# Kernel tuning notes

Hardware: AMD Instinct MI355X
Metric: run time of the kernel (lower is better)

## Reference

```python
import jax, jax.numpy as jnp
import numpy as np

N = 50000      # nodes
E = 800000     # edges
IN = 128       # in_dim
EMB = 32       # emb_dim
ED = 8         # edge_dim
L = 4          # num_layers
B = 64         # num graphs in batch
OUT = 10       # out_dim
EPS = 1e-5


def setup_inputs() -> dict:
    key = jax.random.key(0)
    ks = jax.random.split(key, 16)
    f32 = jnp.float32
    def nrm(k, shape, scale):
        return jax.random.normal(k, shape, dtype=f32) * scale
    inp = {}
    inp['x'] = nrm(ks[0], (N, IN), 1.0)
    inp['edge_index'] = jax.random.randint(ks[1], (2, E), 0, N)
    inp['edge_attr'] = nrm(ks[2], (E, ED), 1.0)
    inp['batch'] = jnp.sort(jax.random.randint(ks[3], (N,), 0, B))
    # lin_in
    inp['lin_in_w'] = nrm(ks[4], (IN, EMB), 0.05)
    inp['lin_in_b'] = jnp.zeros((EMB,), f32)
    # per-layer message MLP: Linear(2e+ed->e), BN, ReLU, Linear(e->e), BN, ReLU
    inp['msg_w1'] = nrm(ks[5], (L, 2 * EMB + ED, EMB), 0.1)
    inp['msg_b1'] = jnp.zeros((L, EMB), f32)
    inp['msg_g1'] = jnp.ones((L, EMB), f32)
    inp['msg_be1'] = jnp.zeros((L, EMB), f32)
    inp['msg_w2'] = nrm(ks[6], (L, EMB, EMB), 0.1)
    inp['msg_b2'] = jnp.zeros((L, EMB), f32)
    inp['msg_g2'] = jnp.ones((L, EMB), f32)
    inp['msg_be2'] = jnp.zeros((L, EMB), f32)
    # per-layer update MLP: Linear(2e->e), BN, ReLU, Linear(e->e), BN, ReLU
    inp['upd_w1'] = nrm(ks[7], (L, 2 * EMB, EMB), 0.1)
    inp['upd_b1'] = jnp.zeros((L, EMB), f32)
    inp['upd_g1'] = jnp.ones((L, EMB), f32)
    inp['upd_be1'] = jnp.zeros((L, EMB), f32)
    inp['upd_w2'] = nrm(ks[8], (L, EMB, EMB), 0.1)
    inp['upd_b2'] = jnp.zeros((L, EMB), f32)
    inp['upd_g2'] = jnp.ones((L, EMB), f32)
    inp['upd_be2'] = jnp.zeros((L, EMB), f32)
    # lin_pred
    inp['pred_w'] = nrm(ks[9], (EMB, OUT), 0.1)
    inp['pred_b'] = jnp.zeros((OUT,), f32)
    return inp


def _bn(x, g, b):
    # BatchNorm1d in training mode: batch stats over dim 0 (biased variance)
    mu = jnp.mean(x, axis=0)
    var = jnp.mean(jnp.square(x - mu), axis=0)
    return (x - mu) * jax.lax.rsqrt(var + EPS) * g + b


def reference(x, edge_attr, lin_in_w, lin_in_b,
              msg_w1, msg_b1, msg_g1, msg_be1, msg_w2, msg_b2, msg_g2, msg_be2,
              upd_w1, upd_b1, upd_g1, upd_be1, upd_w2, upd_b2, upd_g2, upd_be2,
              pred_w, pred_b, edge_index, batch):
    src = edge_index[0]  # h_j source nodes
    dst = edge_index[1]  # h_i target nodes (aggregation index)
    h = x @ lin_in_w + lin_in_b  # [N, EMB]
    for i in range(L):
        # message: gather + concat + MLP(BN,ReLU)x2 over edges
        msg_in = jnp.concatenate([h[dst], h[src], edge_attr], axis=-1)  # [E, 2e+ed]
        m = jax.nn.relu(_bn(msg_in @ msg_w1[i] + msg_b1[i], msg_g1[i], msg_be1[i]))
        m = jax.nn.relu(_bn(m @ msg_w2[i] + msg_b2[i], msg_g2[i], msg_be2[i]))
        # aggregate: scatter-add by destination
        aggr = jax.ops.segment_sum(m, dst, num_segments=N)  # [N, EMB]
        # update: concat + MLP(BN,ReLU)x2
        u = jnp.concatenate([h, aggr], axis=-1)  # [N, 2e]
        u = jax.nn.relu(_bn(u @ upd_w1[i] + upd_b1[i], upd_g1[i], upd_be1[i]))
        u = jax.nn.relu(_bn(u @ upd_w2[i] + upd_b2[i], upd_g2[i], upd_be2[i]))
        h = u + h  # residual in MPNNModel.get_embeddings
    # global mean pool
    sums = jax.ops.segment_sum(h, batch, num_segments=B)
    counts = jax.ops.segment_sum(jnp.ones((N,), h.dtype), batch, num_segments=B)
    h_graph = sums / jnp.maximum(counts, 1.0)[:, None]
    return h_graph @ pred_w + pred_b  # [B, OUT]
```

## Files before the change

kernel.cpp:

```cpp
#include <hip/hip_runtime.h>
#include <cstddef>

#define N_NODES 50000
#define N_EDGES 800000
#define IN_DIM  128
#define EMB     32
#define ED      8
#define NLAYERS 4
#define NB      64
#define OUTD    10
#define EPS_BN  1e-5f

#define EDGE_GRID 3125
#define NODE_GRID 196
#define NODE4_GRID 782
#define AU_GRID   6250
#define NTILE_N   3125
#define LIN_GRID  782
#define ST_TPW    4
#define ST_GRID   3125
#define MSG2_TPW  4
#define MSG2_GRID 3125

#define SREP 4

typedef short bf16x8 __attribute__((ext_vector_type(8)));
typedef float f32x4  __attribute__((ext_vector_type(4)));


__device__ __forceinline__ unsigned short f2bf(float x) {
  union { float f; unsigned u; } v; v.f = x;
  unsigned b = v.u + 0x7FFFu + ((v.u >> 16) & 1u);
  return (unsigned short)(b >> 16);
}
__device__ __forceinline__ float bf2f(unsigned short s) {
  union { unsigned u; float f; } v; v.u = ((unsigned)s) << 16;
  return v.f;
}

__device__ __forceinline__ void coef_from_stats(const float* __restrict__ stats_stage,
                                                const float* __restrict__ g,
                                                const float* __restrict__ be,
                                                float inv_count, float* __restrict__ cf) {
  if (threadIdx.x < EMB) {
    const int c = threadIdx.x;
    float s = 0.f, ss = 0.f;
#pragma unroll
    for (int r = 0; r < SREP; ++r) {
      s  += stats_stage[r*64 + c];
      ss += stats_stage[r*64 + EMB + c];
    }
    const float mu  = s * inv_count;
    const float var = ss * inv_count - mu*mu;
    const float a = g[c] * rsqrtf(var + EPS_BN);
    cf[c] = a;
    cf[EMB + c] = fmaf(-mu, a, be[c]);
  }
  __syncthreads();
}

__device__ __forceinline__ void wave_stats_atomic(float ts[8], float tss[8],
                                                  float* __restrict__ lds_s,
                                                  float* __restrict__ lds_q,
                                                  float* __restrict__ stats_stage) {
  const int lane = threadIdx.x & 63;
  const int wv   = threadIdx.x >> 6;
#pragma unroll
  for (int j = 0; j < 8; ++j) {
    float a = ts[j], b = tss[j];
#pragma unroll
    for (int o = 32; o > 0; o >>= 1) {
      a += __shfl_down(a, o, 64);
      b += __shfl_down(b, o, 64);
    }
    ts[j] = a; tss[j] = b;
  }
  if (lane == 0) {
#pragma unroll
    for (int j = 0; j < 8; ++j) {
      lds_s[wv*8 + j] = ts[j];
      lds_q[wv*8 + j] = tss[j];
    }
  }
  __syncthreads();
  if (threadIdx.x < 64) {
    const float v = (threadIdx.x < 32) ? lds_s[threadIdx.x] : lds_q[threadIdx.x - 32];
    atomicAdd(stats_stage + ((blockIdx.x & (SREP-1)) << 6) + threadIdx.x, v);
  }
}

#define HSTRIDE 40

__global__ __launch_bounds__(256) void k_lin_in_pq(
    const float* __restrict__ x, const float* __restrict__ w, const float* __restrict__ b,
    const float* __restrict__ w1, const float* __restrict__ b1, const int* __restrict__ ei,
    float* __restrict__ h, unsigned short* __restrict__ p, unsigned short* __restrict__ q,
    int* __restrict__ cnt)
{
  __shared__ __align__(16) unsigned short lds_hb[4][16*HSTRIDE];
  __shared__ __align__(16) unsigned short lds_pq[4][16*HSTRIDE];
  const int lane = threadIdx.x & 63;
  const int wv   = threadIdx.x >> 6;
  const int n0i  = lane & 15;
  const int quad = lane >> 4;

  const int tile = blockIdx.x*4 + wv;
  if (tile < NTILE_N) {
    const int r0 = tile*16;
    bf16x8 BwL[4], BwH[4];
#pragma unroll
    for (int kb = 0; kb < 4; ++kb) {
#pragma unroll
      for (int j = 0; j < 8; ++j) {
        const int k = kb*32 + quad*8 + j;
        BwL[kb][j] = (short)f2bf(w[k*EMB + n0i]);
        BwH[kb][j] = (short)f2bf(w[k*EMB + 16 + n0i]);
      }
    }
    f32x4 accL = {0.f,0.f,0.f,0.f};
    f32x4 accH = {0.f,0.f,0.f,0.f};
#pragma unroll
    for (int kb = 0; kb < 4; ++kb) {
      const float4 xa = *(const float4*)(x + (size_t)(r0 + n0i)*IN_DIM + kb*32 + quad*8);
      const float4 xb = *(const float4*)(x + (size_t)(r0 + n0i)*IN_DIM + kb*32 + quad*8 + 4);
      bf16x8 A;
      A[0] = (short)f2bf(xa.x); A[1] = (short)f2bf(xa.y);
      A[2] = (short)f2bf(xa.z); A[3] = (short)f2bf(xa.w);
      A[4] = (short)f2bf(xb.x); A[5] = (short)f2bf(xb.y);
      A[6] = (short)f2bf(xb.z); A[7] = (short)f2bf(xb.w);
      accL = __builtin_amdgcn_mfma_f32_16x16x32_bf16(A, BwL[kb], accL, 0, 0, 0);
      accH = __builtin_amdgcn_mfma_f32_16x16x32_bf16(A, BwH[kb], accH, 0, 0, 0);
    }
    const float bL = b[n0i], bH = b[16 + n0i];
#pragma unroll
    for (int r = 0; r < 4; ++r) {
      const int row = quad*4 + r;
      const float vL = accL[r] + bL;
      const float vH = accH[r] + bH;
      h[(size_t)(r0 + row)*EMB + n0i]      = vL;
      h[(size_t)(r0 + row)*EMB + 16 + n0i] = vH;
      lds_hb[wv][row*HSTRIDE + n0i]      = f2bf(vL);
      lds_hb[wv][row*HSTRIDE + 16 + n0i] = f2bf(vH);
    }
    bf16x8 A2;
#pragma unroll
    for (int j = 0; j < 8; ++j)
      A2[j] = (short)lds_hb[wv][n0i*HSTRIDE + quad*8 + j];
    bf16x8 BpL, BpH, BqL, BqH;
#pragma unroll
    for (int j = 0; j < 8; ++j) {
      const int k = quad*8 + j;
      BpL[j] = (short)f2bf(w1[k*EMB + n0i]);
      BpH[j] = (short)f2bf(w1[k*EMB + 16 + n0i]);
      BqL[j] = (short)f2bf(w1[(EMB + k)*EMB + n0i]);
      BqH[j] = (short)f2bf(w1[(EMB + k)*EMB + 16 + n0i]);
    }
    const f32x4 z4 = {0.f,0.f,0.f,0.f};
    f32x4 pL = __builtin_amdgcn_mfma_f32_16x16x32_bf16(A2, BpL, z4, 0, 0, 0);
    f32x4 pH = __builtin_amdgcn_mfma_f32_16x16x32_bf16(A2, BpH, z4, 0, 0, 0);
    f32x4 qL = __builtin_amdgcn_mfma_f32_16x16x32_bf16(A2, BqL, z4, 0, 0, 0);
    f32x4 qH = __builtin_amdgcn_mfma_f32_16x16x32_bf16(A2, BqH, z4, 0, 0, 0);
    const float b1L = b1[n0i], b1H = b1[16 + n0i];
#pragma unroll
    for (int r = 0; r < 4; ++r) {
      const int row = quad*4 + r;
      lds_pq[wv][row*HSTRIDE + n0i]      = f2bf(pL[r] + b1L);
      lds_pq[wv][row*HSTRIDE + 16 + n0i] = f2bf(pH[r] + b1H);
    }
    {
      const int row2 = lane >> 2;
      const int c8   = (lane & 3)*8;
      const uint4 ov = *(const uint4*)&lds_pq[wv][row2*HSTRIDE + c8];
      *(uint4*)(p + (size_t)(r0 + row2)*EMB + c8) = ov;
    }
#pragma unroll
    for (int r = 0; r < 4; ++r) {
      const int row = quad*4 + r;
      lds_pq[wv][row*HSTRIDE + n0i]      = f2bf(qL[r]);
      lds_pq[wv][row*HSTRIDE + 16 + n0i] = f2bf(qH[r]);
    }
    {
      const int row2 = lane >> 2;
      const int c8   = (lane & 3)*8;
      const uint4 ov = *(const uint4*)&lds_pq[wv][row2*HSTRIDE + c8];
      *(uint4*)(q + (size_t)(r0 + row2)*EMB + c8) = ov;
    }
  }
  for (int e = blockIdx.x*256 + threadIdx.x; e < N_EDGES; e += gridDim.x*256)
    atomicAdd(&cnt[ei[N_EDGES + e]], 1);
}

__global__ __launch_bounds__(256) void k_scan_a(const int* __restrict__ cnt,
                                                int* __restrict__ row_ptr, int* __restrict__ bsum) {
  __shared__ int s[256];
  const int gid = blockIdx.x*256 + threadIdx.x;
  const int v = (gid < N_NODES) ? cnt[gid] : 0;
  s[threadIdx.x] = v;
  __syncthreads();
  for (int o = 1; o < 256; o <<= 1) {
    const int t = (threadIdx.x >= o) ? s[threadIdx.x - o] : 0;
    __syncthreads();
    s[threadIdx.x] += t;
    __syncthreads();
  }
  if (gid < N_NODES) row_ptr[gid] = s[threadIdx.x] - v;
  if (threadIdx.x == 255) bsum[blockIdx.x] = s[255];
}

__global__ __launch_bounds__(256) void k_scan_bc(int* __restrict__ row_ptr,
                                                 const int* __restrict__ bsum) {
  __shared__ int s[256];
  const int t = threadIdx.x;
  const int v = (t < NODE_GRID) ? bsum[t] : 0;
  s[t] = v;
  __syncthreads();
  for (int o = 1; o < 256; o <<= 1) {
    const int tt = (t >= o) ? s[t - o] : 0;
    __syncthreads();
    s[t] += tt;
    __syncthreads();
  }
  const int off = (blockIdx.x == 0) ? 0 : s[blockIdx.x - 1];
  const int gid = blockIdx.x*256 + t;
  if (gid < N_NODES) row_ptr[gid] += off;
  if (blockIdx.x == 0 && t == 0) row_ptr[N_NODES] = N_EDGES;
}

__global__ __launch_bounds__(256) void k_place_scatter(
    const int* __restrict__ ei, const float* __restrict__ ea,
    const int* __restrict__ row_ptr, int* __restrict__ cnt2,
    uint4* __restrict__ rec)
{
  const int e = blockIdx.x*256 + threadIdx.x;
  const int s = ei[e];
  const int d = ei[N_EDGES + e];
  const int pos = row_ptr[d] + atomicAdd(&cnt2[d], 1);
  const float4 v0 = ((const float4*)(ea + (size_t)e*ED))[0];
  const float4 v1 = ((const float4*)(ea + (size_t)e*ED))[1];
  const float ev[8] = {v0.x, v0.y, v0.z, v0.w, v1.x, v1.y, v1.z, v1.w};
  unsigned u[4];
#pragma unroll
  for (int j = 0; j < 4; ++j)
    u[j] = (unsigned)f2bf(ev[2*j]) | ((unsigned)f2bf(ev[2*j+1]) << 16);
  uint4* rp = rec + (size_t)pos*2;
  rp[0] = make_uint4((unsigned)s, (unsigned)d, u[0], u[1]);
  rp[1] = make_uint4(u[2], u[3], 0u, 0u);
}


__global__ __launch_bounds__(256) void k_stats1(
    const unsigned short* __restrict__ pb, const unsigned short* __restrict__ qb,
    const uint4* __restrict__ rec, const float* __restrict__ w1b,
    float* __restrict__ stats)
{
  __shared__ float lds_d[4][16*33];
  __shared__ float lds_s[4][32], lds_q[4][32];
  const int lane = threadIdx.x & 63;
  const int wv   = threadIdx.x >> 6;
  const int l15  = lane & 15;
  const int quad = lane >> 4;

  bf16x8 B1lo = {}, B1hi = {};
  if (quad == 0) {
#pragma unroll
    for (int j = 0; j < 8; ++j) {
      B1lo[j] = (short)f2bf(w1b[j*EMB + l15]);
      B1hi[j] = (short)f2bf(w1b[j*EMB + 16 + l15]);
    }
  }

  const int tile0 = blockIdx.x * (4*ST_TPW);
  uint4 RA[ST_TPW], RB[ST_TPW];
#pragma unroll
  for (int t = 0; t < ST_TPW; ++t) {
    const int tile = tile0 + t*4 + wv;
    const size_t e0 = (size_t)tile * 16;
    const uint4* r4 = rec + (e0 + l15)*2;
    RA[t] = r4[0];
    RB[t] = (quad == 0) ? r4[1] : make_uint4(0u,0u,0u,0u);
  }
  uint4 PG[ST_TPW], QG[ST_TPW];
#pragma unroll
  for (int t = 0; t < ST_TPW; ++t) {
    PG[t] = *(const uint4*)(pb + (size_t)RA[t].y*EMB + quad*8);
    QG[t] = *(const uint4*)(qb + (size_t)RA[t].x*EMB + quad*8);
  }

  float ts[8], tss[8];
#pragma unroll
  for (int j = 0; j < 8; ++j) { ts[j] = 0.f; tss[j] = 0.f; }

#pragma unroll
  for (int t = 0; t < ST_TPW; ++t) {
    bf16x8 A = {};
    if (quad == 0) {
      A[0] = (short)(RA[t].z & 0xFFFFu); A[1] = (short)(RA[t].z >> 16);
      A[2] = (short)(RA[t].w & 0xFFFFu); A[3] = (short)(RA[t].w >> 16);
      A[4] = (short)(RB[t].x & 0xFFFFu); A[5] = (short)(RB[t].x >> 16);
      A[6] = (short)(RB[t].y & 0xFFFFu); A[7] = (short)(RB[t].y >> 16);
    }
    const f32x4 z4 = {0.f,0.f,0.f,0.f};
    f32x4 D0 = __builtin_amdgcn_mfma_f32_16x16x32_bf16(A, B1lo, z4, 0, 0, 0);
    f32x4 D1 = __builtin_amdgcn_mfma_f32_16x16x32_bf16(A, B1hi, z4, 0, 0, 0);
#pragma unroll
    for (int r = 0; r < 4; ++r) {
      const int row = quad*4 + r;
      lds_d[wv][row*33 + l15]      = D0[r];
      lds_d[wv][row*33 + 16 + l15] = D1[r];
    }
    const unsigned pu[4] = {PG[t].x, PG[t].y, PG[t].z, PG[t].w};
    const unsigned qu[4] = {QG[t].x, QG[t].y, QG[t].z, QG[t].w};
#pragma unroll
    for (int jj = 0; jj < 4; ++jj) {
      const float d0 = lds_d[wv][l15*33 + quad*8 + 2*jj];
      const float d1 = lds_d[wv][l15*33 + quad*8 + 2*jj + 1];
      const float v0 = (d0 + bf2f((unsigned short)(pu[jj] & 0xFFFFu)))
                            + bf2f((unsigned short)(qu[jj] & 0xFFFFu));
      const float v1 = (d1 + bf2f((unsigned short)(pu[jj] >> 16)))
                            + bf2f((unsigned short)(qu[jj] >> 16));
      const float w0 = bf2f(f2bf(v0));
      const float w1v = bf2f(f2bf(v1));
      ts[2*jj]   += w0;  tss[2*jj]   = fmaf(w0, w0, tss[2*jj]);
      ts[2*jj+1] += w1v; tss[2*jj+1] = fmaf(w1v, w1v, tss[2*jj+1]);
    }
  }

#pragma unroll
  for (int j = 0; j < 8; ++j) {
    float a = ts[j], b = tss[j];
#pragma unroll
    for (int o = 1; o < 16; o <<= 1) {
      a += __shfl_xor(a, o, 64);
      b += __shfl_xor(b, o, 64);
    }
    ts[j] = a; tss[j] = b;
  }
  if (l15 == 0) {
#pragma unroll
    for (int j = 0; j < 8; ++j) {
      lds_s[wv][quad*8 + j] = ts[j];
      lds_q[wv][quad*8 + j] = tss[j];
    }
  }
  __syncthreads();
  if (threadIdx.x < 64) {
    const int c = threadIdx.x & 31;
    const int kind = threadIdx.x >> 5;
    float v = 0.f;
#pragma unroll
    for (int wq = 0; wq < 4; ++wq)
      v += kind ? lds_q[wq][c] : lds_s[wq][c];
    atomicAdd(stats + ((blockIdx.x & (SREP-1)) << 6) + kind*32 + c, v);
  }
}

__global__ __launch_bounds__(256) void k_msg2(
    const unsigned short* __restrict__ pb, const unsigned short* __restrict__ qb,
    const uint4* __restrict__ rec, const float* __restrict__ w1b,
    const float* __restrict__ stats1, const float* __restrict__ g1, const float* __restrict__ be1,
    const float* __restrict__ w2, const float* __restrict__ b2,
    unsigned short* __restrict__ y, float* __restrict__ stats2)
{
  __shared__ float lds_d[4][16*33];
  __shared__ __align__(16) unsigned short lds_t[4][16*32];
  __shared__ float lds_s[4][32], lds_q[4][32];
  __shared__ float cf[64];

  coef_from_stats(stats1, g1, be1, 1.0f/(float)N_EDGES, cf);

  const int lane = threadIdx.x & 63;
  const int wv   = threadIdx.x >> 6;
  const int l15  = lane & 15;
  const int quad = lane >> 4;

  bf16x8 B1lo = {}, B1hi = {};
  if (quad == 0) {
#pragma unroll
    for (int j = 0; j < 8; ++j) {
      B1lo[j] = (short)f2bf(w1b[j*EMB + l15]);
      B1hi[j] = (short)f2bf(w1b[j*EMB + 16 + l15]);
    }
  }
  bf16x8 Blo, Bhi;
#pragma unroll
  for (int j = 0; j < 8; ++j) {
    Blo[j] = (short)f2bf(w2[(quad*8 + j)*EMB + l15]);
    Bhi[j] = (short)f2bf(w2[(quad*8 + j)*EMB + 16 + l15]);
  }
  float a1[8], c1[8];
#pragma unroll
  for (int j = 0; j < 8; ++j) {
    a1[j] = cf[quad*8 + j];
    c1[j] = cf[EMB + quad*8 + j];
  }
  const float b2c0 = b2[l15], b2c1 = b2[16 + l15];

  float ts[8], tss[8];
#pragma unroll
  for (int j = 0; j < 8; ++j) { ts[j] = 0.f; tss[j] = 0.f; }

  const int tile0 = blockIdx.x * (4*MSG2_TPW);

  uint4 cRA, cRB, cPG, cQG;
  {
    const size_t e0 = (size_t)(tile0 + wv) * 16;
    const uint4* r4 = rec + (e0 + l15)*2;
    cRA = r4[0];
    cRB = (quad == 0) ? r4[1] : make_uint4(0u,0u,0u,0u);
    cPG = *(const uint4*)(pb + (size_t)cRA.y*EMB + quad*8);
    cQG = *(const uint4*)(qb + (size_t)cRA.x*EMB + quad*8);
  }

#pragma unroll
  for (int t = 0; t < MSG2_TPW; ++t) {
    const size_t e0 = (size_t)(tile0 + t*4 + wv) * 16;

    uint4 nRA = make_uint4(0u,0u,0u,0u), nRB = make_uint4(0u,0u,0u,0u);
    uint4 nPG = make_uint4(0u,0u,0u,0u), nQG = make_uint4(0u,0u,0u,0u);
    if (t + 1 < MSG2_TPW) {
      const size_t e1 = (size_t)(tile0 + (t+1)*4 + wv) * 16;
      const uint4* r4 = rec + (e1 + l15)*2;
      nRA = r4[0];
      nRB = (quad == 0) ? r4[1] : make_uint4(0u,0u,0u,0u);
    }

    bf16x8 A = {};
    if (quad == 0) {
      A[0] = (short)(cRA.z & 0xFFFFu); A[1] = (short)(cRA.z >> 16);
      A[2] = (short)(cRA.w & 0xFFFFu); A[3] = (short)(cRA.w >> 16);
      A[4] = (short)(cRB.x & 0xFFFFu); A[5] = (short)(cRB.x >> 16);
      A[6] = (short)(cRB.y & 0xFFFFu); A[7] = (short)(cRB.y >> 16);
    }
    const f32x4 z4 = {0.f,0.f,0.f,0.f};
    f32x4 D0 = __builtin_amdgcn_mfma_f32_16x16x32_bf16(A, B1lo, z4, 0, 0, 0);
    f32x4 D1 = __builtin_amdgcn_mfma_f32_16x16x32_bf16(A, B1hi, z4, 0, 0, 0);
#pragma unroll
    for (int r = 0; r < 4; ++r) {
      const int row = quad*4 + r;
      lds_d[wv][row*33 + l15]      = D0[r];
      lds_d[wv][row*33 + 16 + l15] = D1[r];
    }

    if (t + 1 < MSG2_TPW) {
      nPG = *(const uint4*)(pb + (size_t)nRA.y*EMB + quad*8);
      nQG = *(const uint4*)(qb + (size_t)nRA.x*EMB + quad*8);
    }

    const unsigned pu[4] = {cPG.x, cPG.y, cPG.z, cPG.w};
    const unsigned qu[4] = {cQG.x, cQG.y, cQG.z, cQG.w};
    bf16x8 A2;
#pragma unroll
    for (int jj = 0; jj < 4; ++jj) {
      const float d0 = lds_d[wv][l15*33 + quad*8 + 2*jj];
      const float d1 = lds_d[wv][l15*33 + quad*8 + 2*jj + 1];
      const float v0 = (d0 + bf2f((unsigned short)(pu[jj] & 0xFFFFu)))
                            + bf2f((unsigned short)(qu[jj] & 0xFFFFu));
      const float v1 = (d1 + bf2f((unsigned short)(pu[jj] >> 16)))
                            + bf2f((unsigned short)(qu[jj] >> 16));
      const float w0 = bf2f(f2bf(v0));
      const float w1v = bf2f(f2bf(v1));
      const float r0 = fmaxf(fmaf(a1[2*jj],   w0,  c1[2*jj]),   0.f);
      const float r1 = fmaxf(fmaf(a1[2*jj+1], w1v, c1[2*jj+1]), 0.f);
      A2[2*jj]   = (short)f2bf(r0);
      A2[2*jj+1] = (short)f2bf(r1);
    }

    f32x4 acc0 = {0.f, 0.f, 0.f, 0.f};
    f32x4 acc1 = {0.f, 0.f, 0.f, 0.f};
    acc0 = __builtin_amdgcn_mfma_f32_16x16x32_bf16(A2, Blo, acc0, 0, 0, 0);
    acc1 = __builtin_amdgcn_mfma_f32_16x16x32_bf16(A2, Bhi, acc1, 0, 0, 0);

#pragma unroll
    for (int r = 0; r < 4; ++r) {
      const int row = quad*4 + r;
      lds_t[wv][row*32 + l15]      = f2bf(acc0[r] + b2c0);
      lds_t[wv][row*32 + 16 + l15] = f2bf(acc1[r] + b2c1);
    }
    const uint4 orow = *(const uint4*)&lds_t[wv][(lane>>2)*32 + (lane&3)*8];
    *(uint4*)(y + (e0 + (lane>>2))*EMB + (lane&3)*8) = orow;

    const unsigned uo[4] = {orow.x, orow.y, orow.z, orow.w};
#pragma unroll
    for (int j = 0; j < 4; ++j) {
      const float v0 = bf2f((unsigned short)(uo[j] & 0xFFFFu));
      const float v1 = bf2f((unsigned short)(uo[j] >> 16));
      ts[2*j]   += v0;  tss[2*j]   = fmaf(v0, v0, tss[2*j]);
      ts[2*j+1] += v1;  tss[2*j+1] = fmaf(v1, v1, tss[2*j+1]);
    }

    cRA = nRA; cRB = nRB; cPG = nPG; cQG = nQG;
  }

#pragma unroll
  for (int j = 0; j < 8; ++j) {
    float s = ts[j], qq = tss[j];
#pragma unroll
    for (int o = 4; o < 64; o <<= 1) {
      s  += __shfl_xor(s, o, 64);
      qq += __shfl_xor(qq, o, 64);
    }
    ts[j] = s; tss[j] = qq;
  }
  if (lane < 4) {
#pragma unroll
    for (int j = 0; j < 8; ++j) {
      lds_s[wv][lane*8 + j] = ts[j];
      lds_q[wv][lane*8 + j] = tss[j];
    }
  }
  __syncthreads();
  if (threadIdx.x < 64) {
    const int c = threadIdx.x & 31;
    const int kind = threadIdx.x >> 5;
    float v = 0.f;
#pragma unroll
    for (int wq = 0; wq < 4; ++wq)
      v += kind ? lds_q[wq][c] : lds_s[wq][c];
    atomicAdd(stats2 + ((blockIdx.x & (SREP-1)) << 6) + kind*32 + c, v);
  }
}

__global__ __launch_bounds__(256) void k_aggr_upd1(
    const unsigned short* __restrict__ y, const int* __restrict__ row_ptr,
    const float* __restrict__ h,
    const float* __restrict__ stats1, const float* __restrict__ g2, const float* __restrict__ be2,
    const float* __restrict__ uw1, const float* __restrict__ ub1,
    float* __restrict__ z, float* __restrict__ stats2)
{
  __shared__ float cf[64];
  __shared__ float lh[8][32];
  __shared__ float la[8][32];
  __shared__ float rs[4][32], rq[4][32];
  coef_from_stats(stats1, g2, be2, 1.0f/(float)N_EDGES, cf);

  const int g = threadIdx.x >> 5;
  const int l = threadIdx.x & 31;
  const int n = blockIdx.x*8 + g;

  lh[g][l] = h[(size_t)n*EMB + l];

  const int c8  = (l & 3) * 8;
  const int rof = l >> 2;
  float a[8], b[8];
#pragma unroll
  for (int j = 0; j < 8; ++j) { a[j] = cf[c8 + j]; b[j] = cf[EMB + c8 + j]; }
  const int lo = row_ptr[n], hi = row_ptr[n+1];
  float acc[8];
#pragma unroll
  for (int j = 0; j < 8; ++j) acc[j] = 0.f;
  for (int r = lo + rof; r < hi; r += 8) {
    const uint4 u = *(const uint4*)(y + (size_t)r*EMB + c8);
    const unsigned uu[4] = {u.x, u.y, u.z, u.w};
#pragma unroll
    for (int t = 0; t < 4; ++t) {
      const float v0 = bf2f((unsigned short)(uu[t] & 0xFFFFu));
      const float v1 = bf2f((unsigned short)(uu[t] >> 16));
      acc[2*t]   += fmaxf(fmaf(a[2*t],   v0, b[2*t]),   0.f);
      acc[2*t+1] += fmaxf(fmaf(a[2*t+1], v1, b[2*t+1]), 0.f);
    }
  }
#pragma unroll
  for (int j = 0; j < 8; ++j) {
    float v = acc[j];
    v += __shfl_xor(v, 4, 64);
    v += __shfl_xor(v, 8, 64);
    v += __shfl_xor(v, 16, 64);
    acc[j] = v;
  }
  if (rof == 0) {
#pragma unroll
    for (int j = 0; j < 8; ++j) la[g][c8 + j] = acc[j];
  }
  __syncthreads();

  float accu = ub1[l];
#pragma unroll
  for (int k = 0; k < EMB; ++k) accu = fmaf(lh[g][k], uw1[k*EMB + l], accu);
#pragma unroll
  for (int k = 0; k < EMB; ++k) accu = fmaf(la[g][k], uw1[(EMB + k)*EMB + l], accu);
  z[(size_t)n*EMB + l] = accu;

  const float sq = accu*accu;
  const float a2 = accu + __shfl_down(accu, 32, 64);
  const float q2 = sq   + __shfl_down(sq,   32, 64);
  const int wv = threadIdx.x >> 6;
  if ((threadIdx.x & 63) < 32) { rs[wv][l] = a2; rq[wv][l] = q2; }
  __syncthreads();
  if (threadIdx.x < 64) {
    const int c = threadIdx.x & 31;
    const int kind = threadIdx.x >> 5;
    float v = 0.f;
#pragma unroll
    for (int wq = 0; wq < 4; ++wq)
      v += kind ? rq[wq][c] : rs[wq][c];
    atomicAdd(stats2 + ((blockIdx.x & (SREP-1)) << 6) + kind*32 + c, v);
  }
}

__global__ __launch_bounds__(256) void k_upd2(
    float* __restrict__ z,
    const float* __restrict__ stats1, const float* __restrict__ g1, const float* __restrict__ be1,
    const float* __restrict__ w, const float* __restrict__ b,
    float* __restrict__ stats2)
{
  __shared__ float cf[64];
  __shared__ float lds_s[32], lds_q[32];
  coef_from_stats(stats1, g1, be1, 1.0f/(float)N_NODES, cf);

  const int lane = threadIdx.x & 63;
  const int wv   = threadIdx.x >> 6;
  const int n  = blockIdx.x*64 + lane;
  const int c0 = wv*8;
  float acc[8];
#pragma unroll
  for (int j = 0; j < 8; ++j) acc[j] = 0.f;
  if (n < N_NODES) {
#pragma unroll
    for (int j = 0; j < 8; ++j) acc[j] = b[c0 + j];
    const float4* zp = (const float4*)(z + (size_t)n*EMB);
#pragma unroll
    for (int k4 = 0; k4 < 8; ++k4) {
      const float4 v = zp[k4];
      const float mv[4] = {v.x, v.y, v.z, v.w};
#pragma unroll
      for (int t = 0; t < 4; ++t) {
        const int k = 4*k4 + t;
        const float m = fmaxf(fmaf(cf[k], mv[t], cf[EMB + k]), 0.f);
        const float* wk = w + k*EMB + c0;
#pragma unroll
        for (int j = 0; j < 8; ++j) acc[j] = fmaf(m, wk[j], acc[j]);
      }
    }
  }
  float ts[8], tss[8];
#pragma unroll
  for (int j = 0; j < 8; ++j) { ts[j] = acc[j]; tss[j] = acc[j]*acc[j]; }
  wave_stats_atomic(ts, tss, lds_s, lds_q, stats2);
  if (n < N_NODES) {
    float4 o0, o1;
    o0.x = acc[0]; o0.y = acc[1]; o0.z = acc[2]; o0.w = acc[3];
    o1.x = acc[4]; o1.y = acc[5]; o1.z = acc[6]; o1.w = acc[7];
    *(float4*)(z + (size_t)n*EMB + c0)     = o0;
    *(float4*)(z + (size_t)n*EMB + c0 + 4) = o1;
  }
}

__global__ __launch_bounds__(256) void k_resid_pq(
    float* __restrict__ h, const float* __restrict__ z,
    const float* __restrict__ stats, const float* __restrict__ g, const float* __restrict__ be,
    const float* __restrict__ w1_next, const float* __restrict__ b1_next,
    unsigned short* __restrict__ p, unsigned short* __restrict__ q)
{
  __shared__ float cf[64];
  __shared__ float lds_h[64][33];
  coef_from_stats(stats, g, be, 1.0f/(float)N_NODES, cf);

  const int lane = threadIdx.x & 63;
  const int wv   = threadIdx.x >> 6;
  const int n  = blockIdx.x*64 + lane;
  const int c0 = wv*8;
  if (n < N_NODES) {
    const float4* zp = (const float4*)(z + (size_t)n*EMB + c0);
    float4* hp = (float4*)(h + (size_t)n*EMB + c0);
    float hn[8];
    const float4 z0 = zp[0], z1 = zp[1];
    const float4 h0 = hp[0], h1 = hp[1];
    const float zv[8] = {z0.x, z0.y, z0.z, z0.w, z1.x, z1.y, z1.z, z1.w};
    const float hv[8] = {h0.x, h0.y, h0.z, h0.w, h1.x, h1.y, h1.z, h1.w};
#pragma unroll
    for (int j = 0; j < 8; ++j) {
      const int k = c0 + j;
      hn[j] = hv[j] + fmaxf(fmaf(cf[k], zv[j], cf[EMB + k]), 0.f);
      lds_h[lane][k] = hn[j];
    }
    float4 o0, o1;
    o0.x = hn[0]; o0.y = hn[1]; o0.z = hn[2]; o0.w = hn[3];
    o1.x = hn[4]; o1.y = hn[5]; o1.z = hn[6]; o1.w = hn[7];
    hp[0] = o0; hp[1] = o1;
  }
  __syncthreads();
  if (n < N_NODES && w1_next) {
    float ap[8], aq[8];
#pragma unroll
    for (int j = 0; j < 8; ++j) { ap[j] = b1_next[c0 + j]; aq[j] = 0.f; }
#pragma unroll
    for (int k = 0; k < EMB; ++k) {
      const float hvv = lds_h[lane][k];
      const float* wp = w1_next + k*EMB + c0;
      const float* wq = w1_next + (EMB + k)*EMB + c0;
#pragma unroll
      for (int j = 0; j < 8; ++j) ap[j] = fmaf(hvv, wp[j], ap[j]);
#pragma unroll
      for (int j = 0; j < 8; ++j) aq[j] = fmaf(hvv, wq[j], aq[j]);
    }
    unsigned up[4], uq[4];
#pragma unroll
    for (int j = 0; j < 4; ++j) {
      up[j] = (unsigned)f2bf(ap[2*j]) | ((unsigned)f2bf(ap[2*j+1]) << 16);
      uq[j] = (unsigned)f2bf(aq[2*j]) | ((unsigned)f2bf(aq[2*j+1]) << 16);
    }
    uint4 op; op.x = up[0]; op.y = up[1]; op.z = up[2]; op.w = up[3];
    uint4 oq; oq.x = uq[0]; oq.y = uq[1]; oq.z = uq[2]; oq.w = uq[3];
    *(uint4*)(p + (size_t)n*EMB + c0) = op;
    *(uint4*)(q + (size_t)n*EMB + c0) = oq;
  }
}

__global__ void k_pool(const float* __restrict__ h, const int* __restrict__ batch,
                       const float* __restrict__ pw, const float* __restrict__ pb,
                       float* __restrict__ out)
{
  __shared__ float sred[256];
  __shared__ float hg[EMB];
  const int b = blockIdx.x;
  int lo = 0, hi = N_NODES;
  while (lo < hi) { int m = (lo + hi) >> 1; if (batch[m] < b) lo = m + 1; else hi = m; }
  const int start = lo;
  hi = N_NODES;
  while (lo < hi) { int m = (lo + hi) >> 1; if (batch[m] < b + 1) lo = m + 1; else hi = m; }
  const int end = lo;

  const int c = threadIdx.x & (EMB-1);
  const int r = threadIdx.x >> 5;
  float s = 0.f;
  for (int n = start + r; n < end; n += 8) s += h[(size_t)n*EMB + c];
  sred[threadIdx.x] = s;
  __syncthreads();
  if (threadIdx.x < EMB) {
    float tot = 0.f;
#pragma unroll
    for (int r2 = 0; r2 < 8; ++r2) tot += sred[r2*EMB + threadIdx.x];
    const float cnt = (float)(end - start);
    hg[threadIdx.x] = tot / fmaxf(cnt, 1.f);
  }
  __syncthreads();
  if (threadIdx.x < OUTD) {
    float acc = pb[threadIdx.x];
#pragma unroll
    for (int cc = 0; cc < EMB; ++cc) acc = fmaf(hg[cc], pw[cc*OUTD + threadIdx.x], acc);
    out[b*OUTD + threadIdx.x] = acc;
  }
}


extern "C" void kernel_launch(void* const* d_in, const int* in_sizes, int n_in,
                              void* d_out, int out_size, void* d_ws, size_t ws_size,
                              hipStream_t stream) {
  const float* x        = (const float*)d_in[0];
  const int*   ei       = (const int*)  d_in[1];
  const float* ea       = (const float*)d_in[2];
  const int*   batch    = (const int*)  d_in[3];
  const float* lin_in_w = (const float*)d_in[4];
  const float* lin_in_b = (const float*)d_in[5];
  const float* msg_w1   = (const float*)d_in[6];
  const float* msg_b1   = (const float*)d_in[7];
  const float* msg_g1   = (const float*)d_in[8];
  const float* msg_be1  = (const float*)d_in[9];
  const float* msg_w2   = (const float*)d_in[10];
  const float* msg_b2   = (const float*)d_in[11];
  const float* msg_g2   = (const float*)d_in[12];
  const float* msg_be2  = (const float*)d_in[13];
  const float* upd_w1   = (const float*)d_in[14];
  const float* upd_b1   = (const float*)d_in[15];
  const float* upd_g1   = (const float*)d_in[16];
  const float* upd_be1  = (const float*)d_in[17];
  const float* upd_w2   = (const float*)d_in[18];
  const float* upd_b2   = (const float*)d_in[19];
  const float* upd_g2   = (const float*)d_in[20];
  const float* upd_be2  = (const float*)d_in[21];
  const float* pred_w   = (const float*)d_in[22];
  const float* pred_b   = (const float*)d_in[23];
  float* out = (float*)d_out;

  char* wsb = (char*)d_ws;
  unsigned short* y  = (unsigned short*)wsb;
  uint4* rec = (uint4*)(wsb + (size_t)N_EDGES*EMB*2);
  unsigned short* p  = (unsigned short*)(rec + (size_t)N_EDGES*2);
  unsigned short* q  = p + (size_t)N_NODES*EMB;
  float* h       = (float*)(q + (size_t)N_NODES*EMB);
  float* z       = h + (size_t)N_NODES*EMB;
  float* stats   = z + (size_t)N_NODES*EMB;
  int*   cnt     = (int*)(stats + 16*SREP*64);
  int*   cnt2    = cnt + N_NODES;
  int*   row_ptr = cnt2 + N_NODES;
  int*   bsum    = row_ptr + N_NODES + 1;
  const size_t need = ((size_t)((char*)(bsum + 256) - wsb));
  if (ws_size < need) return;

  hipMemsetAsync(stats, 0, (16*SREP*64 + 2*N_NODES)*sizeof(float), stream);

  k_lin_in_pq<<<LIN_GRID, 256, 0, stream>>>(x, lin_in_w, lin_in_b, msg_w1, msg_b1, ei,
                                            h, p, q, cnt);
  k_scan_a<<<NODE_GRID, 256, 0, stream>>>(cnt, row_ptr, bsum);
  k_scan_bc<<<NODE_GRID, 256, 0, stream>>>(row_ptr, bsum);
  k_place_scatter<<<EDGE_GRID, 256, 0, stream>>>(ei, ea, row_ptr, cnt2, rec);

  for (int l = 0; l < NLAYERS; ++l) {
    const int st = l*4;
    const float* w1  = msg_w1 + (size_t)l*(2*EMB+ED)*EMB;
    const float* w1b = w1 + (size_t)2*EMB*EMB;
    const float* w2  = msg_w2 + (size_t)l*EMB*EMB;
    const float* uw1 = upd_w1 + (size_t)l*(2*EMB)*EMB;
    const float* uw2 = upd_w2 + (size_t)l*EMB*EMB;
    const float* w1_next = (l+1 < NLAYERS) ? msg_w1 + (size_t)(l+1)*(2*EMB+ED)*EMB : nullptr;
    const float* b1_next = (l+1 < NLAYERS) ? msg_b1 + (size_t)(l+1)*EMB : nullptr;

    k_stats1<<<ST_GRID, 256, 0, stream>>>(p, q, rec, w1b, stats + (size_t)st*SREP*64);
    k_msg2<<<MSG2_GRID, 256, 0, stream>>>(p, q, rec, w1b,
                                          stats + (size_t)st*SREP*64,
                                          msg_g1 + l*EMB, msg_be1 + l*EMB,
                                          w2, msg_b2 + l*EMB,
                                          y, stats + (size_t)(st+1)*SREP*64);
    k_aggr_upd1<<<AU_GRID, 256, 0, stream>>>(y, row_ptr, h,
                                             stats + (size_t)(st+1)*SREP*64,
                                             msg_g2 + l*EMB, msg_be2 + l*EMB,
                                             uw1, upd_b1 + l*EMB,
                                             z, stats + (size_t)(st+2)*SREP*64);
    k_upd2<<<NODE4_GRID, 256, 0, stream>>>(z, stats + (size_t)(st+2)*SREP*64,
                                           upd_g1 + l*EMB, upd_be1 + l*EMB,
                                           uw2, upd_b2 + l*EMB, stats + (size_t)(st+3)*SREP*64);
    k_resid_pq<<<NODE4_GRID, 256, 0, stream>>>(h, z, stats + (size_t)(st+3)*SREP*64,
                                               upd_g2 + l*EMB, upd_be2 + l*EMB,
                                               w1_next, b1_next, p, q);
  }

  k_pool<<<NB, 256, 0, stream>>>(h, batch, pred_w, pred_b, out);
}
```

Before: 820.2 us.

## Keep edge records in original order and aggregate via inverse permutation

Edge records (src, dst, bf16 edge attributes) are now built in original edge order inside the lin_in kernel, instead of being scattered into dst-sorted positions in a separate pass. The placement kernel now only writes an inverse permutation array, and the aggregation kernel reads each message row through that index. The x loads in lin_in are also hoisted ahead of the weight conversion. This saves the scattered 32-byte record writes during preprocessing. In exchange, the per-layer message kernels lose the dst locality of sorted records, and aggregation becomes an indirect gather of message rows.

```diff
diff --git a/kernel.cpp b/kernel.cpp
--- a/kernel.cpp
+++ b/kernel.cpp
@@ -94,8 +94,9 @@
 __global__ __launch_bounds__(256) void k_lin_in_pq(
     const float* __restrict__ x, const float* __restrict__ w, const float* __restrict__ b,
     const float* __restrict__ w1, const float* __restrict__ b1, const int* __restrict__ ei,
+    const float* __restrict__ ea,
     float* __restrict__ h, unsigned short* __restrict__ p, unsigned short* __restrict__ q,
-    int* __restrict__ cnt)
+    int* __restrict__ cnt, uint4* __restrict__ rec)
 {
   __shared__ __align__(16) unsigned short lds_hb[4][16*HSTRIDE];
   __shared__ __align__(16) unsigned short lds_pq[4][16*HSTRIDE];
@@ -107,6 +108,12 @@
   const int tile = blockIdx.x*4 + wv;
   if (tile < NTILE_N) {
     const int r0 = tile*16;
+    float4 xa[4], xb[4];
+#pragma unroll
+    for (int kb = 0; kb < 4; ++kb) {
+      xa[kb] = *(const float4*)(x + (size_t)(r0 + n0i)*IN_DIM + kb*32 + quad*8);
+      xb[kb] = *(const float4*)(x + (size_t)(r0 + n0i)*IN_DIM + kb*32 + quad*8 + 4);
+    }
     bf16x8 BwL[4], BwH[4];
 #pragma unroll
     for (int kb = 0; kb < 4; ++kb) {
@@ -121,13 +128,11 @@
     f32x4 accH = {0.f,0.f,0.f,0.f};
 #pragma unroll
     for (int kb = 0; kb < 4; ++kb) {
-      const float4 xa = *(const float4*)(x + (size_t)(r0 + n0i)*IN_DIM + kb*32 + quad*8);
-      const float4 xb = *(const float4*)(x + (size_t)(r0 + n0i)*IN_DIM + kb*32 + quad*8 + 4);
       bf16x8 A;
-      A[0] = (short)f2bf(xa.x); A[1] = (short)f2bf(xa.y);
-      A[2] = (short)f2bf(xa.z); A[3] = (short)f2bf(xa.w);
-      A[4] = (short)f2bf(xb.x); A[5] = (short)f2bf(xb.y);
-      A[6] = (short)f2bf(xb.z); A[7] = (short)f2bf(xb.w);
+      A[0] = (short)f2bf(xa[kb].x); A[1] = (short)f2bf(xa[kb].y);
+      A[2] = (short)f2bf(xa[kb].z); A[3] = (short)f2bf(xa[kb].w);
+      A[4] = (short)f2bf(xb[kb].x); A[5] = (short)f2bf(xb[kb].y);
+      A[6] = (short)f2bf(xb[kb].z); A[7] = (short)f2bf(xb[kb].w);
       accL = __builtin_amdgcn_mfma_f32_16x16x32_bf16(A, BwL[kb], accL, 0, 0, 0);
       accH = __builtin_amdgcn_mfma_f32_16x16x32_bf16(A, BwH[kb], accH, 0, 0, 0);
     }
@@ -186,8 +191,21 @@
       *(uint4*)(q + (size_t)(r0 + row2)*EMB + c8) = ov;
     }
   }
-  for (int e = blockIdx.x*256 + threadIdx.x; e < N_EDGES; e += gridDim.x*256)
-    atomicAdd(&cnt[ei[N_EDGES + e]], 1);
+  for (int e = blockIdx.x*256 + threadIdx.x; e < N_EDGES; e += gridDim.x*256) {
+    const int s = ei[e];
+    const int d = ei[N_EDGES + e];
+    atomicAdd(&cnt[d], 1);
+    const float4 v0 = ((const float4*)(ea + (size_t)e*ED))[0];
+    const float4 v1 = ((const float4*)(ea + (size_t)e*ED))[1];
+    const float ev[8] = {v0.x, v0.y, v0.z, v0.w, v1.x, v1.y, v1.z, v1.w};
+    unsigned u[4];
+#pragma unroll
+    for (int j = 0; j < 4; ++j)
+      u[j] = (unsigned)f2bf(ev[2*j]) | ((unsigned)f2bf(ev[2*j+1]) << 16);
+    uint4* rp = rec + (size_t)e*2;
+    rp[0] = make_uint4((unsigned)s, (unsigned)d, u[0], u[1]);
+    rp[1] = make_uint4(u[2], u[3], 0u, 0u);
+  }
 }
 
 __global__ __launch_bounds__(256) void k_scan_a(const int* __restrict__ cnt,
@@ -226,25 +244,14 @@
   if (blockIdx.x == 0 && t == 0) row_ptr[N_NODES] = N_EDGES;
 }
 
-__global__ __launch_bounds__(256) void k_place_scatter(
-    const int* __restrict__ ei, const float* __restrict__ ea,
-    const int* __restrict__ row_ptr, int* __restrict__ cnt2,
-    uint4* __restrict__ rec)
+__global__ __launch_bounds__(256) void k_place(
+    const int* __restrict__ ei, const int* __restrict__ row_ptr, int* __restrict__ cnt2,
+    int* __restrict__ inv)
 {
   const int e = blockIdx.x*256 + threadIdx.x;
-  const int s = ei[e];
   const int d = ei[N_EDGES + e];
   const int pos = row_ptr[d] + atomicAdd(&cnt2[d], 1);
-  const float4 v0 = ((const float4*)(ea + (size_t)e*ED))[0];
-  const float4 v1 = ((const float4*)(ea + (size_t)e*ED))[1];
-  const float ev[8] = {v0.x, v0.y, v0.z, v0.w, v1.x, v1.y, v1.z, v1.w};
-  unsigned u[4];
-#pragma unroll
-  for (int j = 0; j < 4; ++j)
-    u[j] = (unsigned)f2bf(ev[2*j]) | ((unsigned)f2bf(ev[2*j+1]) << 16);
-  uint4* rp = rec + (size_t)pos*2;
-  rp[0] = make_uint4((unsigned)s, (unsigned)d, u[0], u[1]);
-  rp[1] = make_uint4(u[2], u[3], 0u, 0u);
+  inv[pos] = e;
 }
 
 
@@ -522,6 +529,7 @@
 
 __global__ __launch_bounds__(256) void k_aggr_upd1(
     const unsigned short* __restrict__ y, const int* __restrict__ row_ptr,
+    const int* __restrict__ inv,
     const float* __restrict__ h,
     const float* __restrict__ stats1, const float* __restrict__ g2, const float* __restrict__ be2,
     const float* __restrict__ uw1, const float* __restrict__ ub1,
@@ -549,7 +557,8 @@
 #pragma unroll
   for (int j = 0; j < 8; ++j) acc[j] = 0.f;
   for (int r = lo + rof; r < hi; r += 8) {
-    const uint4 u = *(const uint4*)(y + (size_t)r*EMB + c8);
+    const int ee = inv[r];
+    const uint4 u = *(const uint4*)(y + (size_t)ee*EMB + c8);
     const unsigned uu[4] = {u.x, u.y, u.z, u.w};
 #pragma unroll
     for (int t = 0; t < 4; ++t) {
@@ -784,16 +793,17 @@
   int*   cnt2    = cnt + N_NODES;
   int*   row_ptr = cnt2 + N_NODES;
   int*   bsum    = row_ptr + N_NODES + 1;
-  const size_t need = ((size_t)((char*)(bsum + 256) - wsb));
+  int*   inv     = bsum + 256;
+  const size_t need = ((size_t)((char*)(inv + N_EDGES) - wsb));
   if (ws_size < need) return;
 
   hipMemsetAsync(stats, 0, (16*SREP*64 + 2*N_NODES)*sizeof(float), stream);
 
-  k_lin_in_pq<<<LIN_GRID, 256, 0, stream>>>(x, lin_in_w, lin_in_b, msg_w1, msg_b1, ei,
-                                            h, p, q, cnt);
+  k_lin_in_pq<<<LIN_GRID, 256, 0, stream>>>(x, lin_in_w, lin_in_b, msg_w1, msg_b1, ei, ea,
+                                            h, p, q, cnt, rec);
   k_scan_a<<<NODE_GRID, 256, 0, stream>>>(cnt, row_ptr, bsum);
   k_scan_bc<<<NODE_GRID, 256, 0, stream>>>(row_ptr, bsum);
-  k_place_scatter<<<EDGE_GRID, 256, 0, stream>>>(ei, ea, row_ptr, cnt2, rec);
+  k_place<<<EDGE_GRID, 256, 0, stream>>>(ei, row_ptr, cnt2, inv);
 
   for (int l = 0; l < NLAYERS; ++l) {
     const int st = l*4;
@@ -811,7 +821,7 @@
                                           msg_g1 + l*EMB, msg_be1 + l*EMB,
                                           w2, msg_b2 + l*EMB,
                                           y, stats + (size_t)(st+1)*SREP*64);
-    k_aggr_upd1<<<AU_GRID, 256, 0, stream>>>(y, row_ptr, h,
+    k_aggr_upd1<<<AU_GRID, 256, 0, stream>>>(y, row_ptr, inv, h,
                                              stats + (size_t)(st+1)*SREP*64,
                                              msg_g2 + l*EMB, msg_be2 + l*EMB,
                                              uw1, upd_b1 + l*EMB,
```

After: 851.3 us. 3.8% more time.
